# Optimization experiments

Hardware: AMD Instinct MI355X
Metric: run time of the kernel (lower is better)

Reference implementation:

```python
import jax, jax.numpy as jnp
import numpy as np

NUM_CLASSES = 8192
BRANCHING = 8
BATCH = 8192
DEPTH_PARAM = 0.1
EPS = 1e-8


def _build_tree():
    """Synthetic 8-ary tree over NUM_CLASSES nodes (node 0 is root).
    Returns padded leaf->root paths [C, D] and path lengths [C]."""
    C = NUM_CLASSES
    parent = np.zeros(C, dtype=np.int64)
    parent[1:] = (np.arange(1, C) - 1) // BRANCHING
    cur = np.arange(C)
    cols = [cur.copy()]
    lens = np.ones(C, dtype=np.int32)
    alive = cur > 0
    while alive.any():
        cur = np.where(alive, parent[cur], cur)
        cols.append(cur.copy())
        lens += alive.astype(np.int32)
        alive = cur > 0
    paths = np.stack(cols, axis=1).astype(np.int32)  # [C, D]; padded cells repeat root
    return paths, lens


def setup_inputs() -> dict:
    key = jax.random.key(0)
    k1, k2 = jax.random.split(key)
    y_pred = jax.random.normal(k1, (BATCH, NUM_CLASSES), dtype=jnp.float32)
    y_true = jax.random.uniform(k2, (BATCH, NUM_CLASSES), dtype=jnp.float32)
    paths_np, lens_np = _build_tree()
    rng = np.random.default_rng(0)
    counts = rng.integers(1, 1000, size=NUM_CLASSES).astype(np.float64)
    class_w = (counts.max() / counts).astype(np.float32)
    return {
        "y_pred": y_pred,
        "y_true": y_true,
        "class_w": jnp.asarray(class_w),
        "tree_paths": jnp.asarray(paths_np),
        "tree_lens": jnp.asarray(lens_np),
    }


def reference(y_pred, y_true, class_w, tree_paths, tree_lens):
    # p: softmax over class dim
    p = jax.nn.softmax(y_pred, axis=1)                       # [B, C]
    labels = jnp.argmax(y_true, axis=1)                      # [B]
    paths = tree_paths[labels]                               # [B, D] leaf->root ids
    lens = tree_lens[labels]                                 # [B]
    B, D = paths.shape
    probs = jnp.take_along_axis(p, paths, axis=1)            # [B, D]
    k = jnp.arange(D)
    node_mask = k[None, :] < lens[:, None]
    probs = jnp.where(node_mask, probs, 0.0)
    # suffix sums: s[:, k] = sum_{j>=k} probs[:, j]  (node + all its ancestors)
    s = jnp.cumsum(probs[:, ::-1], axis=1)[:, ::-1]          # [B, D]
    s_next = jnp.concatenate([s[:, 1:], jnp.zeros((B, 1), s.dtype)], axis=1)
    cond = s / (s_next + EPS)                                # conditional prob per level
    height = (lens[:, None] - 1 - k[None, :]).astype(p.dtype)
    w = jnp.exp(-DEPTH_PARAM * height)                       # depth weighting
    valid = k[None, :] < (lens[:, None] - 1)                 # levels 0..L-2
    path_loss = jnp.sum(jnp.where(valid, w * jnp.log(cond + EPS), 0.0), axis=1)
    loss = jnp.mean(-class_w[labels] * path_loss)
    return loss
```

## Files before the change

### kernel.cpp

```cpp
#include <hip/hip_runtime.h>
#include <math.h>

#define BLOCK 256
#define MAX_D 16
#define EPS 1e-8f
#define DEPTH_PARAM 0.1f

__global__ __launch_bounds__(BLOCK) void chcel_kernel(
    const float* __restrict__ y_pred,
    const float* __restrict__ y_true,
    const float* __restrict__ class_w,
    const int* __restrict__ paths,
    const int* __restrict__ lens,
    float* __restrict__ out,
    int C, int D, float invB)
{
    const int row  = blockIdx.x;
    const int tid  = threadIdx.x;
    const int lane = tid & 63;
    const int wid  = tid >> 6;

    const float4* yp4 = (const float4*)(y_pred + (size_t)row * C);
    const float4* yt4 = (const float4*)(y_true + (size_t)row * C);

    float4 a[8];
    float m  = -INFINITY;
    float tv = -INFINITY;
    int   ti = 0x7fffffff;
    #pragma unroll
    for (int j = 0; j < 8; ++j) {
        const int v = tid + j * BLOCK;
        a[j] = yp4[v];
        m = fmaxf(m, fmaxf(fmaxf(a[j].x, a[j].y), fmaxf(a[j].z, a[j].w)));
        float4 t = yt4[v];
        const int base = v << 2;
        if (t.x > tv) { tv = t.x; ti = base;     }
        if (t.y > tv) { tv = t.y; ti = base + 1; }
        if (t.z > tv) { tv = t.z; ti = base + 2; }
        if (t.w > tv) { tv = t.w; ti = base + 3; }
    }

    #pragma unroll
    for (int off = 32; off; off >>= 1) {
        m = fmaxf(m, __shfl_xor(m, off, 64));
        float ov = __shfl_xor(tv, off, 64);
        int   oi = __shfl_xor(ti, off, 64);
        if (ov > tv || (ov == tv && oi < ti)) { tv = ov; ti = oi; }
    }

    __shared__ float sm[4];
    __shared__ float stv[4];
    __shared__ int   sti[4];
    __shared__ float ss[4];
    if (lane == 0) { sm[wid] = m; stv[wid] = tv; sti[wid] = ti; }
    __syncthreads();

    const float M = fmaxf(fmaxf(sm[0], sm[1]), fmaxf(sm[2], sm[3]));

    float s = 0.f;
    #pragma unroll
    for (int j = 0; j < 8; ++j) {
        s += __expf(a[j].x - M) + __expf(a[j].y - M)
           + __expf(a[j].z - M) + __expf(a[j].w - M);
    }
    #pragma unroll
    for (int off = 32; off; off >>= 1) s += __shfl_xor(s, off, 64);
    if (lane == 0) ss[wid] = s;
    __syncthreads();

    if (tid == 0) {
        const float S = ss[0] + ss[1] + ss[2] + ss[3];

        float bv = stv[0]; int bi = sti[0];
        #pragma unroll
        for (int w = 1; w < 4; ++w) {
            if (stv[w] > bv || (stv[w] == bv && sti[w] < bi)) { bv = stv[w]; bi = sti[w]; }
        }
        const int label = bi;
        const int len   = lens[label];

        const float* yp = y_pred + (size_t)row * C;
        float probs[MAX_D];
        for (int k = 0; k < len && k < MAX_D; ++k) {
            const int node = paths[(size_t)label * D + k];
            probs[k] = __expf(yp[node] - M) / S;
        }

        float suffix = 0.f, acc = 0.f;
        for (int k = len - 1; k >= 0; --k) {
            const float s_next = suffix;
            suffix += probs[k];
            if (k <= len - 2) {
                const float h = (float)(len - 1 - k);
                acc += __expf(-DEPTH_PARAM * h) * __logf(suffix / (s_next + EPS) + EPS);
            }
        }
        atomicAdd(out, -class_w[label] * acc * invB);
    }
}

extern "C" void kernel_launch(void* const* d_in, const int* in_sizes, int n_in,
                              void* d_out, int out_size, void* d_ws, size_t ws_size,
                              hipStream_t stream) {
    const float* y_pred  = (const float*)d_in[0];
    const float* y_true  = (const float*)d_in[1];
    const float* class_w = (const float*)d_in[2];
    const int*   paths   = (const int*)d_in[3];
    const int*   lens    = (const int*)d_in[4];
    float* out = (float*)d_out;

    const int C = in_sizes[2];
    const int B = in_sizes[0] / C;
    const int D = in_sizes[3] / C;
    const float invB = 1.0f / (float)B;

    hipMemsetAsync(out, 0, sizeof(float) * out_size, stream);
    chcel_kernel<<<B, BLOCK, 0, stream>>>(y_pred, y_true, class_w, paths, lens,
                                          out, C, D, invB);
}
```

Baseline: 526.6 us.

## Use online softmax with two accumulators and replace atomic with reduce kernel

Computes max and sum-of-exponentials in one pass with an online-softmax rescale, using two independent accumulator chains. This removes the need to keep the row's 32 floats in registers across a second pass and the extra barrier. The single-address atomicAdd and the memset are replaced by per-row writes to workspace plus a one-block reduction kernel, which makes the sum deterministic. In exchange it issues more exp calls and adds a second kernel launch.

```diff
diff --git a/kernel.cpp b/kernel.cpp
--- a/kernel.cpp
+++ b/kernel.cpp
@@ -6,14 +6,14 @@
 #define EPS 1e-8f
 #define DEPTH_PARAM 0.1f
 
-__global__ __launch_bounds__(BLOCK) void chcel_kernel(
+__global__ __launch_bounds__(BLOCK) void chcel_row_kernel(
     const float* __restrict__ y_pred,
     const float* __restrict__ y_true,
     const float* __restrict__ class_w,
     const int* __restrict__ paths,
     const int* __restrict__ lens,
-    float* __restrict__ out,
-    int C, int D, float invB)
+    float* __restrict__ rowloss,
+    int C, int D)
 {
     const int row  = blockIdx.x;
     const int tid  = threadIdx.x;
@@ -23,53 +23,78 @@
     const float4* yp4 = (const float4*)(y_pred + (size_t)row * C);
     const float4* yt4 = (const float4*)(y_true + (size_t)row * C);
 
-    float4 a[8];
-    float m  = -INFINITY;
+    float m0 = -INFINITY, s0 = 0.f;
+    float m1 = -INFINITY, s1 = 0.f;
     float tv = -INFINITY;
     int   ti = 0x7fffffff;
+
     #pragma unroll
-    for (int j = 0; j < 8; ++j) {
-        const int v = tid + j * BLOCK;
-        a[j] = yp4[v];
-        m = fmaxf(m, fmaxf(fmaxf(a[j].x, a[j].y), fmaxf(a[j].z, a[j].w)));
-        float4 t = yt4[v];
-        const int base = v << 2;
-        if (t.x > tv) { tv = t.x; ti = base;     }
-        if (t.y > tv) { tv = t.y; ti = base + 1; }
-        if (t.z > tv) { tv = t.z; ti = base + 2; }
-        if (t.w > tv) { tv = t.w; ti = base + 3; }
+    for (int j = 0; j < 8; j += 2) {
+        const int v0 = tid + j * BLOCK;
+        const int v1 = tid + (j + 1) * BLOCK;
+        float4 a0 = yp4[v0];
+        float4 a1 = yp4[v1];
+        float4 t0 = yt4[v0];
+        float4 t1 = yt4[v1];
+
+        float c  = fmaxf(fmaxf(a0.x, a0.y), fmaxf(a0.z, a0.w));
+        float nm = fmaxf(m0, c);
+        s0 = s0 * __expf(m0 - nm)
+           + __expf(a0.x - nm) + __expf(a0.y - nm)
+           + __expf(a0.z - nm) + __expf(a0.w - nm);
+        m0 = nm;
+        c  = fmaxf(fmaxf(a1.x, a1.y), fmaxf(a1.z, a1.w));
+        nm = fmaxf(m1, c);
+        s1 = s1 * __expf(m1 - nm)
+           + __expf(a1.x - nm) + __expf(a1.y - nm)
+           + __expf(a1.z - nm) + __expf(a1.w - nm);
+        m1 = nm;
+
+        int base = v0 << 2;
+        if (t0.x > tv) { tv = t0.x; ti = base;     }
+        if (t0.y > tv) { tv = t0.y; ti = base + 1; }
+        if (t0.z > tv) { tv = t0.z; ti = base + 2; }
+        if (t0.w > tv) { tv = t0.w; ti = base + 3; }
+        base = v1 << 2;
+        if (t1.x > tv) { tv = t1.x; ti = base;     }
+        if (t1.y > tv) { tv = t1.y; ti = base + 1; }
+        if (t1.z > tv) { tv = t1.z; ti = base + 2; }
+        if (t1.w > tv) { tv = t1.w; ti = base + 3; }
+    }
+
+    {
+        const float M = fmaxf(m0, m1);
+        s0 = s0 * __expf(m0 - M) + s1 * __expf(m1 - M);
+        m0 = M;
     }
 
     #pragma unroll
     for (int off = 32; off; off >>= 1) {
-        m = fmaxf(m, __shfl_xor(m, off, 64));
-        float ov = __shfl_xor(tv, off, 64);
-        int   oi = __shfl_xor(ti, off, 64);
+        const float om = __shfl_xor(m0, off, 64);
+        const float os = __shfl_xor(s0, off, 64);
+        const float M  = fmaxf(m0, om);
+        s0 = s0 * __expf(m0 - M) + os * __expf(om - M);
+        m0 = M;
+        const float ov = __shfl_xor(tv, off, 64);
+        const int   oi = __shfl_xor(ti, off, 64);
         if (ov > tv || (ov == tv && oi < ti)) { tv = ov; ti = oi; }
     }
 
     __shared__ float sm[4];
+    __shared__ float ssum[4];
     __shared__ float stv[4];
     __shared__ int   sti[4];
-    __shared__ float ss[4];
-    if (lane == 0) { sm[wid] = m; stv[wid] = tv; sti[wid] = ti; }
-    __syncthreads();
-
-    const float M = fmaxf(fmaxf(sm[0], sm[1]), fmaxf(sm[2], sm[3]));
-
-    float s = 0.f;
-    #pragma unroll
-    for (int j = 0; j < 8; ++j) {
-        s += __expf(a[j].x - M) + __expf(a[j].y - M)
-           + __expf(a[j].z - M) + __expf(a[j].w - M);
-    }
-    #pragma unroll
-    for (int off = 32; off; off >>= 1) s += __shfl_xor(s, off, 64);
-    if (lane == 0) ss[wid] = s;
+    if (lane == 0) { sm[wid] = m0; ssum[wid] = s0; stv[wid] = tv; sti[wid] = ti; }
     __syncthreads();
 
     if (tid == 0) {
-        const float S = ss[0] + ss[1] + ss[2] + ss[3];
+        float M = sm[0], S = ssum[0];
+        #pragma unroll
+        for (int w = 1; w < 4; ++w) {
+            const float Mn = fmaxf(M, sm[w]);
+            S = S * __expf(M - Mn) + ssum[w] * __expf(sm[w] - Mn);
+            M = Mn;
+        }
 
         float bv = stv[0]; int bi = sti[0];
         #pragma unroll
@@ -95,8 +120,25 @@
                 acc += __expf(-DEPTH_PARAM * h) * __logf(suffix / (s_next + EPS) + EPS);
             }
         }
-        atomicAdd(out, -class_w[label] * acc * invB);
+        rowloss[row] = -class_w[label] * acc;
     }
+}
+
+__global__ __launch_bounds__(BLOCK) void chcel_reduce_kernel(
+    const float* __restrict__ rowloss, float* __restrict__ out,
+    int B, float invB)
+{
+    const int tid  = threadIdx.x;
+    const int lane = tid & 63;
+    const int wid  = tid >> 6;
+    float s = 0.f;
+    for (int i = tid; i < B; i += BLOCK) s += rowloss[i];
+    #pragma unroll
+    for (int off = 32; off; off >>= 1) s += __shfl_xor(s, off, 64);
+    __shared__ float sb[4];
+    if (lane == 0) sb[wid] = s;
+    __syncthreads();
+    if (tid == 0) out[0] = (sb[0] + sb[1] + sb[2] + sb[3]) * invB;
 }
 
 extern "C" void kernel_launch(void* const* d_in, const int* in_sizes, int n_in,
@@ -108,13 +150,14 @@
     const int*   paths   = (const int*)d_in[3];
     const int*   lens    = (const int*)d_in[4];
     float* out = (float*)d_out;
+    float* rowloss = (float*)d_ws;
 
     const int C = in_sizes[2];
     const int B = in_sizes[0] / C;
     const int D = in_sizes[3] / C;
     const float invB = 1.0f / (float)B;
 
-    hipMemsetAsync(out, 0, sizeof(float) * out_size, stream);
-    chcel_kernel<<<B, BLOCK, 0, stream>>>(y_pred, y_true, class_w, paths, lens,
-                                          out, C, D, invB);
+    chcel_row_kernel<<<B, BLOCK, 0, stream>>>(y_pred, y_true, class_w, paths, lens,
+                                              rowloss, C, D);
+    chcel_reduce_kernel<<<1, BLOCK, 0, stream>>>(rowloss, out, B, invB);
 }
```

Result: no change. 518.8 us (-1.5%).

## Process one row per wavefront with prefetched nontemporal loads and two-stage reduction

Applied to the files above, without the earlier changes.

Each 64-lane wavefront now handles a whole row instead of one 256-thread block per row. Loads are software-pipelined: the next chunk is fetched with nontemporal loads while the current one is processed. The softmax max pass is dropped, so exp is taken on raw logits in a single pass; this removes a reduction and a block sync but can overflow for large logits. The per-lane path gather is shuffle-based, per-row losses go to workspace, and a small second kernel reduces them, replacing the memset plus atomics.

```diff
diff --git a/kernel.cpp b/kernel.cpp
--- a/kernel.cpp
+++ b/kernel.cpp
@@ -2,101 +2,122 @@
 #include <math.h>
 
 #define BLOCK 256
-#define MAX_D 16
 #define EPS 1e-8f
 #define DEPTH_PARAM 0.1f
 
-__global__ __launch_bounds__(BLOCK) void chcel_kernel(
+typedef float f32x4 __attribute__((ext_vector_type(4)));
+
+__device__ __forceinline__ f32x4 ntload(const f32x4* p) {
+    return __builtin_nontemporal_load(p);
+}
+
+__global__ __launch_bounds__(BLOCK, 4) void chcel_row_kernel(
     const float* __restrict__ y_pred,
     const float* __restrict__ y_true,
     const float* __restrict__ class_w,
     const int* __restrict__ paths,
     const int* __restrict__ lens,
-    float* __restrict__ out,
-    int C, int D, float invB)
+    float* __restrict__ rowloss,
+    int C, int D, int B)
 {
-    const int row  = blockIdx.x;
-    const int tid  = threadIdx.x;
-    const int lane = tid & 63;
-    const int wid  = tid >> 6;
+    const int lane = threadIdx.x & 63;
+    const int wave = threadIdx.x >> 6;
+    const int row  = (blockIdx.x << 2) + wave;
+    if (row >= B) return;
 
-    const float4* yp4 = (const float4*)(y_pred + (size_t)row * C);
-    const float4* yt4 = (const float4*)(y_true + (size_t)row * C);
+    const f32x4* yp4 = (const f32x4*)(y_pred + (size_t)row * C);
+    const f32x4* yt4 = (const f32x4*)(y_true + (size_t)row * C);
+    const int nf4   = C >> 2;
+    const int nstep = nf4 >> 8;
 
-    float4 a[8];
-    float m  = -INFINITY;
-    float tv = -INFINITY;
-    int   ti = 0x7fffffff;
+    float sacc[4] = {0.f, 0.f, 0.f, 0.f};
+    float tv[4]; int ti[4];
     #pragma unroll
-    for (int j = 0; j < 8; ++j) {
-        const int v = tid + j * BLOCK;
-        a[j] = yp4[v];
-        m = fmaxf(m, fmaxf(fmaxf(a[j].x, a[j].y), fmaxf(a[j].z, a[j].w)));
-        float4 t = yt4[v];
-        const int base = v << 2;
-        if (t.x > tv) { tv = t.x; ti = base;     }
-        if (t.y > tv) { tv = t.y; ti = base + 1; }
-        if (t.z > tv) { tv = t.z; ti = base + 2; }
-        if (t.w > tv) { tv = t.w; ti = base + 3; }
+    for (int q = 0; q < 4; ++q) { tv[q] = -INFINITY; ti[q] = 0x7fffffff; }
+
+    f32x4 P[4], T[4];
+    #pragma unroll
+    for (int q = 0; q < 4; ++q) {
+        P[q] = ntload(yp4 + lane + (q << 6));
+        T[q] = ntload(yt4 + lane + (q << 6));
+    }
+
+    for (int s = 0; s < nstep; ++s) {
+        f32x4 Pn[4], Tn[4];
+        if (s + 1 < nstep) {
+            const int base = ((s + 1) << 8) + lane;
+            #pragma unroll
+            for (int q = 0; q < 4; ++q) {
+                Pn[q] = ntload(yp4 + base + (q << 6));
+                Tn[q] = ntload(yt4 + base + (q << 6));
+            }
+        }
+        const int ebase = (((s << 8) + lane) << 2);
+        #pragma unroll
+        for (int q = 0; q < 4; ++q) {
+            const f32x4 p = P[q];
+            sacc[q] += (__expf(p.x) + __expf(p.y)) + (__expf(p.z) + __expf(p.w));
+            const f32x4 t = T[q];
+            const int bidx = ebase + (q << 8);
+            if (t.x > tv[q]) { tv[q] = t.x; ti[q] = bidx;     }
+            if (t.y > tv[q]) { tv[q] = t.y; ti[q] = bidx + 1; }
+            if (t.z > tv[q]) { tv[q] = t.z; ti[q] = bidx + 2; }
+            if (t.w > tv[q]) { tv[q] = t.w; ti[q] = bidx + 3; }
+        }
+        #pragma unroll
+        for (int q = 0; q < 4; ++q) { P[q] = Pn[q]; T[q] = Tn[q]; }
+    }
+
+    float S = (sacc[0] + sacc[1]) + (sacc[2] + sacc[3]);
+    float btv = tv[0]; int bti = ti[0];
+    #pragma unroll
+    for (int q = 1; q < 4; ++q) {
+        if (tv[q] > btv || (tv[q] == btv && ti[q] < bti)) { btv = tv[q]; bti = ti[q]; }
     }
 
     #pragma unroll
     for (int off = 32; off; off >>= 1) {
-        m = fmaxf(m, __shfl_xor(m, off, 64));
-        float ov = __shfl_xor(tv, off, 64);
-        int   oi = __shfl_xor(ti, off, 64);
-        if (ov > tv || (ov == tv && oi < ti)) { tv = ov; ti = oi; }
+        S += __shfl_xor(S, off, 64);
+        const float ov = __shfl_xor(btv, off, 64);
+        const int   oi = __shfl_xor(bti, off, 64);
+        if (ov > btv || (ov == btv && oi < bti)) { btv = ov; bti = oi; }
     }
 
-    __shared__ float sm[4];
-    __shared__ float stv[4];
-    __shared__ int   sti[4];
-    __shared__ float ss[4];
-    if (lane == 0) { sm[wid] = m; stv[wid] = tv; sti[wid] = ti; }
-    __syncthreads();
+    const int label = bti;
+    const int len   = lens[label];
+    float prob = 0.f;
+    if (lane < len) {
+        const int node = paths[(size_t)label * D + lane];
+        prob = __expf(y_pred[(size_t)row * C + node]) / S;
+    }
+    float suffix = 0.f, acc = 0.f;
+    for (int k = len - 1; k >= 0; --k) {
+        const float pk = __shfl(prob, k, 64);
+        const float s_next = suffix;
+        suffix += pk;
+        if (k <= len - 2) {
+            const float h = (float)(len - 1 - k);
+            acc += __expf(-DEPTH_PARAM * h) * __logf(suffix / (s_next + EPS) + EPS);
+        }
+    }
+    if (lane == 0) rowloss[row] = -class_w[label] * acc;
+}
 
-    const float M = fmaxf(fmaxf(sm[0], sm[1]), fmaxf(sm[2], sm[3]));
-
+__global__ __launch_bounds__(BLOCK) void chcel_reduce_kernel(
+    const float* __restrict__ rowloss, float* __restrict__ out,
+    int B, float invB)
+{
+    const int tid  = threadIdx.x;
+    const int lane = tid & 63;
+    const int wid  = tid >> 6;
     float s = 0.f;
-    #pragma unroll
-    for (int j = 0; j < 8; ++j) {
-        s += __expf(a[j].x - M) + __expf(a[j].y - M)
-           + __expf(a[j].z - M) + __expf(a[j].w - M);
-    }
+    for (int i = tid; i < B; i += BLOCK) s += rowloss[i];
     #pragma unroll
     for (int off = 32; off; off >>= 1) s += __shfl_xor(s, off, 64);
-    if (lane == 0) ss[wid] = s;
+    __shared__ float sb[4];
+    if (lane == 0) sb[wid] = s;
     __syncthreads();
-
-    if (tid == 0) {
-        const float S = ss[0] + ss[1] + ss[2] + ss[3];
-
-        float bv = stv[0]; int bi = sti[0];
-        #pragma unroll
-        for (int w = 1; w < 4; ++w) {
-            if (stv[w] > bv || (stv[w] == bv && sti[w] < bi)) { bv = stv[w]; bi = sti[w]; }
-        }
-        const int label = bi;
-        const int len   = lens[label];
-
-        const float* yp = y_pred + (size_t)row * C;
-        float probs[MAX_D];
-        for (int k = 0; k < len && k < MAX_D; ++k) {
-            const int node = paths[(size_t)label * D + k];
-            probs[k] = __expf(yp[node] - M) / S;
-        }
-
-        float suffix = 0.f, acc = 0.f;
-        for (int k = len - 1; k >= 0; --k) {
-            const float s_next = suffix;
-            suffix += probs[k];
-            if (k <= len - 2) {
-                const float h = (float)(len - 1 - k);
-                acc += __expf(-DEPTH_PARAM * h) * __logf(suffix / (s_next + EPS) + EPS);
-            }
-        }
-        atomicAdd(out, -class_w[label] * acc * invB);
-    }
+    if (tid == 0) out[0] = (sb[0] + sb[1] + sb[2] + sb[3]) * invB;
 }
 
 extern "C" void kernel_launch(void* const* d_in, const int* in_sizes, int n_in,
@@ -108,13 +129,15 @@
     const int*   paths   = (const int*)d_in[3];
     const int*   lens    = (const int*)d_in[4];
     float* out = (float*)d_out;
+    float* rowloss = (float*)d_ws;
 
     const int C = in_sizes[2];
     const int B = in_sizes[0] / C;
     const int D = in_sizes[3] / C;
     const float invB = 1.0f / (float)B;
 
-    hipMemsetAsync(out, 0, sizeof(float) * out_size, stream);
-    chcel_kernel<<<B, BLOCK, 0, stream>>>(y_pred, y_true, class_w, paths, lens,
-                                          out, C, D, invB);
+    const int grid = (B + 3) / 4;
+    chcel_row_kernel<<<grid, BLOCK, 0, stream>>>(y_pred, y_true, class_w, paths, lens,
+                                                 rowloss, C, D, B);
+    chcel_reduce_kernel<<<1, BLOCK, 0, stream>>>(rowloss, out, B, invB);
 }
```

After: 485.4 us. 7.8% less time.
